# Performance work log

Measured on AMD Instinct MI355X. Metric: run time of the kernel, lower is better.

## Reference

```python
import jax, jax.numpy as jnp
import numpy as np

EPS_LOG = 1e-8
EPS_CHECK = 1e-4


def to_float8(x, exp_bits=4, mant_bits=3):
    # fp8 emulation: sign/abs/log2/floor/clamp/round chain
    max_exp = 2 ** (exp_bits - 1) - 1
    min_exp = -max_exp
    scale = 2.0 ** mant_bits
    sign = jnp.sign(x)
    x_abs = jnp.abs(x)
    exp = jnp.clip(jnp.floor(jnp.log2(x_abs + EPS_LOG)), min_exp, max_exp)
    pow2 = jnp.exp2(exp)
    mant = x_abs / pow2 - 1.0
    mant_q = jnp.round(mant * scale) / scale
    return sign * (1.0 + mant_q) * pow2


def checksum_verify(left, right, epsilon=EPS_CHECK):
    # ABFT: augment left with a column-sum row, right with a row-sum column
    left_cs = jnp.concatenate([left, jnp.sum(left, axis=0, keepdims=True)], axis=0)
    right_cs = jnp.concatenate([right, jnp.sum(right, axis=1, keepdims=True)], axis=1)
    prod_cs = left_cs @ right_cs  # [(m+1), (n+1)]
    output = prod_cs[:-1, :-1]
    row_sum_check = prod_cs[:-1, -1]
    col_sum_check = prod_cs[-1, :-1]
    col_diff = jnp.abs(jnp.sum(output, axis=0) - col_sum_check)
    row_diff = jnp.abs(jnp.sum(output, axis=1) - row_sum_check)
    mask = (row_diff > epsilon)[:, None] & (col_diff > epsilon)[None, :]
    return output, mask


def setup_inputs() -> dict:
    key = jax.random.key(0)
    kx, ku, kA, kB, kC = jax.random.split(key, 5)
    batch, n, m, p = 4096, 2048, 1024, 1024
    return {
        "x": jax.random.normal(kx, (batch, n), dtype=jnp.float32),
        "u": jax.random.normal(ku, (batch, m), dtype=jnp.float32),
        "A": jax.random.normal(kA, (n, n), dtype=jnp.float32),
        "B": jax.random.normal(kB, (n, m), dtype=jnp.float32),
        "C": jax.random.normal(kC, (p, n), dtype=jnp.float32),
    }


def reference(x, u, A, B, C):
    int_bits, frac_bits = 4, 3
    Aq = to_float8(A, int_bits, frac_bits)
    Bq = to_float8(B, int_bits, frac_bits)
    left_term, left_mask = checksum_verify(x, Aq.T)
    right_term, right_mask = checksum_verify(u, Bq.T)
    x_next = to_float8(left_term + right_term, int_bits, frac_bits)
    _ = left_mask | right_mask  # mask computed but discarded in forward (as in torch)
    Cq = to_float8(C, int_bits, frac_bits)
    y = to_float8(x_next @ Cq.T, int_bits, frac_bits)
    return (x_next, y)
```

## Files before the change

kernel.cpp:

```cpp
#include <hip/hip_runtime.h>
#include <hip/hip_bf16.h>
#include <stdint.h>

typedef __bf16 bf16_t;
typedef __attribute__((ext_vector_type(8))) __bf16 bf16x8;
typedef __attribute__((ext_vector_type(4))) __bf16 bf16x4;
typedef __attribute__((ext_vector_type(4))) float f32x4;

__device__ __forceinline__ float q8(float v) {
    float a = __builtin_fabsf(v);
    float z = a + 1e-8f;
    int ei = ((__float_as_int(z) >> 23) & 0xff) - 127;
    ei = ei > 7 ? 7 : (ei < -7 ? -7 : ei);
    float p  = __int_as_float((ei + 127) << 23);
    float ip = __int_as_float((127 - ei) << 23);
    float m  = __builtin_fmaf(a, ip, -1.0f);
    float mq = __builtin_rintf(m * 8.0f) * 0.125f;
    float r  = (1.0f + mq) * p;
    return v < 0.0f ? -r : r;
}

__device__ __forceinline__ void gload_lds16(const bf16_t* g, bf16_t* l) {
    __builtin_amdgcn_global_load_lds(
        (__attribute__((address_space(1))) void*)(g),
        (__attribute__((address_space(3))) void*)(l), 16, 0, 0);
}

__global__ void pack_all(const float* __restrict__ x, const float* __restrict__ u,
                         const float* __restrict__ A, const float* __restrict__ B,
                         const float* __restrict__ C,
                         bf16_t* __restrict__ XU, bf16_t* __restrict__ AB,
                         bf16_t* __restrict__ CQ) {
    int z = blockIdx.z;
    int row = blockIdx.y;
    int col = (blockIdx.x * 256 + threadIdx.x) * 4;
    if (z == 0) {
        float4 v;
        if (col < 2048) v = *(const float4*)&x[(size_t)row * 2048 + col];
        else            v = *(const float4*)&u[(size_t)row * 1024 + (col - 2048)];
        bf16x4 o = { (bf16_t)v.x, (bf16_t)v.y, (bf16_t)v.z, (bf16_t)v.w };
        *(bf16x4*)&XU[(size_t)row * 3072 + col] = o;
    } else if (z == 1) {
        if (row >= 2048) return;
        float4 v;
        if (col < 2048) v = *(const float4*)&A[(size_t)row * 2048 + col];
        else            v = *(const float4*)&B[(size_t)row * 1024 + (col - 2048)];
        bf16x4 o = { (bf16_t)q8(v.x), (bf16_t)q8(v.y), (bf16_t)q8(v.z), (bf16_t)q8(v.w) };
        *(bf16x4*)&AB[(size_t)row * 3072 + col] = o;
    } else {
        if (row >= 1024 || col >= 2048) return;
        float4 v = *(const float4*)&C[(size_t)row * 2048 + col];
        bf16x4 o = { (bf16_t)q8(v.x), (bf16_t)q8(v.y), (bf16_t)q8(v.z), (bf16_t)q8(v.w) };
        *(bf16x4*)&CQ[(size_t)row * 2048 + col] = o;
    }
}

template<int BN, bool DUAL>
__global__ __launch_bounds__(512, 4)
void gemm_q8_kernel(const bf16_t* __restrict__ A, const bf16_t* __restrict__ B,
                    float* __restrict__ outf, bf16_t* __restrict__ outb,
                    int M, int N, int K) {
    constexpr int BM = 128;
    constexpr int BK = 64;
    constexpr int NI = BN / 32;
    constexpr int A_ITS = BM * BK * 2 / 16 / 512;
    constexpr int B_ITS = BN * BK * 2 / 16 / 512;

    __shared__ alignas(16) bf16_t sA[BM * BK];
    __shared__ alignas(16) bf16_t sB[BN * BK];

    const int tid  = threadIdx.x;
    const int lane = tid & 63;
    const int wave = tid >> 6;
    const int wm   = wave & 3;
    const int wn   = wave >> 2;
    const int ln16 = lane & 15;
    const int quad = lane >> 4;

    const int brow = blockIdx.y * BM;
    const int bcol = blockIdx.x * BN;

    const bf16_t* gA[A_ITS]; bf16_t* lA[A_ITS];
#pragma unroll
    for (int it = 0; it < A_ITS; ++it) {
        int chunk = it * 512 + tid;
        int r  = chunk >> 3;
        int cg = (chunk & 7) ^ (r & 7);
        gA[it] = A + (size_t)(brow + r) * K + cg * 8;
        lA[it] = sA + (it * 512 + wave * 64) * 8;
    }
    const bf16_t* gB[B_ITS]; bf16_t* lB[B_ITS];
#pragma unroll
    for (int it = 0; it < B_ITS; ++it) {
        int chunk = it * 512 + tid;
        int r  = chunk >> 3;
        int cg = (chunk & 7) ^ (r & 7);
        gB[it] = B + (size_t)(bcol + r) * K + cg * 8;
        lB[it] = sB + (it * 512 + wave * 64) * 8;
    }

    int a_off[2][2], b_off[NI][2];
#pragma unroll
    for (int im = 0; im < 2; ++im) {
        int r = wm * 32 + im * 16 + ln16;
#pragma unroll
        for (int s = 0; s < 2; ++s) {
            int cg = s * 4 + quad;
            a_off[im][s] = (r * 8 + (cg ^ (r & 7))) * 8;
        }
    }
#pragma unroll
    for (int in = 0; in < NI; ++in) {
        int r = wn * (BN / 2) + in * 16 + ln16;
#pragma unroll
        for (int s = 0; s < 2; ++s) {
            int cg = s * 4 + quad;
            b_off[in][s] = (r * 8 + (cg ^ (r & 7))) * 8;
        }
    }

    f32x4 acc[2][NI];
#pragma unroll
    for (int im = 0; im < 2; ++im)
#pragma unroll
        for (int in = 0; in < NI; ++in)
            acc[im][in] = (f32x4){0.f, 0.f, 0.f, 0.f};

    for (int kt = 0; kt < K; kt += BK) {
#pragma unroll
        for (int it = 0; it < A_ITS; ++it) gload_lds16(gA[it], lA[it]);
#pragma unroll
        for (int it = 0; it < B_ITS; ++it) gload_lds16(gB[it], lB[it]);
#pragma unroll
        for (int it = 0; it < A_ITS; ++it) gA[it] += BK;
#pragma unroll
        for (int it = 0; it < B_ITS; ++it) gB[it] += BK;
        __syncthreads();
#pragma unroll
        for (int s = 0; s < 2; ++s) {
            bf16x8 af[2], bfv[NI];
#pragma unroll
            for (int im = 0; im < 2; ++im) af[im]  = *(const bf16x8*)(sA + a_off[im][s]);
#pragma unroll
            for (int in = 0; in < NI; ++in) bfv[in] = *(const bf16x8*)(sB + b_off[in][s]);
#pragma unroll
            for (int im = 0; im < 2; ++im)
#pragma unroll
                for (int in = 0; in < NI; ++in)
                    acc[im][in] = __builtin_amdgcn_mfma_f32_16x16x32_bf16(
                        af[im], bfv[in], acc[im][in], 0, 0, 0);
        }
        __syncthreads();
    }

    const int rbase = quad * 4;
#pragma unroll
    for (int im = 0; im < 2; ++im) {
#pragma unroll
        for (int in = 0; in < NI; ++in) {
            int gm = brow + wm * 32 + im * 16 + rbase;
            int gn = bcol + wn * (BN / 2) + in * 16 + ln16;
#pragma unroll
            for (int r = 0; r < 4; ++r) {
                float v = q8(acc[im][in][r]);
                outf[(size_t)(gm + r) * N + gn] = v;
                if (DUAL) outb[(size_t)(gm + r) * N + gn] = (bf16_t)v;
            }
        }
    }
}

extern "C" void kernel_launch(void* const* d_in, const int* in_sizes, int n_in,
                              void* d_out, int out_size, void* d_ws, size_t ws_size,
                              hipStream_t stream) {
    const float* x = (const float*)d_in[0];
    const float* u = (const float*)d_in[1];
    const float* A = (const float*)d_in[2];
    const float* B = (const float*)d_in[3];
    const float* C = (const float*)d_in[4];

    float* outf = (float*)d_out;
    float* xnf  = outf;
    float* yf   = outf + (size_t)4096 * 2048;

    uint8_t* ws = (uint8_t*)d_ws;
    bf16_t* XU = (bf16_t*)ws;
    bf16_t* AB = (bf16_t*)(ws + (size_t)25165824);
    bf16_t* CQ = (bf16_t*)(ws + (size_t)25165824 + 12582912);
    bf16_t* XN = (bf16_t*)(ws + (size_t)25165824 + 12582912 + 4194304);

    pack_all<<<dim3(3, 4096, 3), 256, 0, stream>>>(x, u, A, B, C, XU, AB, CQ);

    gemm_q8_kernel<128, true><<<dim3(2048 / 128, 4096 / 128), 512, 0, stream>>>(
        XU, AB, xnf, XN, 4096, 2048, 3072);
    gemm_q8_kernel<64, false><<<dim3(1024 / 64, 4096 / 128), 512, 0, stream>>>(
        XN, CQ, yf, nullptr, 4096, 1024, 2048);
}
```

Before: 218.8 us.

## Double GEMM K-tile to 128 and flatten pack grid to skip idle blocks

The GEMM K tile grows from 64 to 128, with the XOR swizzle widened to 16 column groups to match the larger row stride. This halves the number of barrier pairs per K loop and doubles the MFMA work between syncs, at the cost of twice the LDS per block, which may lower occupancy. Separately, the pack kernel's 3D grid, where many z=1/z=2 blocks returned immediately, becomes a 1D grid sized to exactly the useful blocks. That avoids launching empty workgroups.

```diff
diff --git a/kernel.cpp b/kernel.cpp
--- a/kernel.cpp
+++ b/kernel.cpp
@@ -31,24 +31,28 @@
                          const float* __restrict__ C,
                          bf16_t* __restrict__ XU, bf16_t* __restrict__ AB,
                          bf16_t* __restrict__ CQ) {
-    int z = blockIdx.z;
-    int row = blockIdx.y;
-    int col = (blockIdx.x * 256 + threadIdx.x) * 4;
-    if (z == 0) {
+    unsigned bid = blockIdx.x;
+    if (bid < 12288u) {
+        unsigned row = bid / 3u, piece = bid - row * 3u;
+        int col = (piece * 256 + threadIdx.x) * 4;
         float4 v;
         if (col < 2048) v = *(const float4*)&x[(size_t)row * 2048 + col];
         else            v = *(const float4*)&u[(size_t)row * 1024 + (col - 2048)];
         bf16x4 o = { (bf16_t)v.x, (bf16_t)v.y, (bf16_t)v.z, (bf16_t)v.w };
         *(bf16x4*)&XU[(size_t)row * 3072 + col] = o;
-    } else if (z == 1) {
-        if (row >= 2048) return;
+    } else if (bid < 18432u) {
+        unsigned b = bid - 12288u;
+        unsigned row = b / 3u, piece = b - row * 3u;
+        int col = (piece * 256 + threadIdx.x) * 4;
         float4 v;
         if (col < 2048) v = *(const float4*)&A[(size_t)row * 2048 + col];
         else            v = *(const float4*)&B[(size_t)row * 1024 + (col - 2048)];
         bf16x4 o = { (bf16_t)q8(v.x), (bf16_t)q8(v.y), (bf16_t)q8(v.z), (bf16_t)q8(v.w) };
         *(bf16x4*)&AB[(size_t)row * 3072 + col] = o;
     } else {
-        if (row >= 1024 || col >= 2048) return;
+        unsigned b = bid - 18432u;
+        unsigned row = b >> 1, piece = b & 1u;
+        int col = (piece * 256 + threadIdx.x) * 4;
         float4 v = *(const float4*)&C[(size_t)row * 2048 + col];
         bf16x4 o = { (bf16_t)q8(v.x), (bf16_t)q8(v.y), (bf16_t)q8(v.z), (bf16_t)q8(v.w) };
         *(bf16x4*)&CQ[(size_t)row * 2048 + col] = o;
@@ -61,10 +65,10 @@
                     float* __restrict__ outf, bf16_t* __restrict__ outb,
                     int M, int N, int K) {
     constexpr int BM = 128;
-    constexpr int BK = 64;
+    constexpr int BK = 128;
     constexpr int NI = BN / 32;
-    constexpr int A_ITS = BM * BK * 2 / 16 / 512;
-    constexpr int B_ITS = BN * BK * 2 / 16 / 512;
+    constexpr int A_ITS = BM * (BK / 8) / 512;
+    constexpr int B_ITS = BN * (BK / 8) / 512;
 
     __shared__ alignas(16) bf16_t sA[BM * BK];
     __shared__ alignas(16) bf16_t sB[BN * BK];
@@ -83,39 +87,37 @@
     const bf16_t* gA[A_ITS]; bf16_t* lA[A_ITS];
 #pragma unroll
     for (int it = 0; it < A_ITS; ++it) {
-        int chunk = it * 512 + tid;
-        int r  = chunk >> 3;
-        int cg = (chunk & 7) ^ (r & 7);
-        gA[it] = A + (size_t)(brow + r) * K + cg * 8;
+        int L = it * 512 + tid;
+        int r = L >> 4, c = L & 15;
+        gA[it] = A + (size_t)(brow + r) * K + (c ^ (r & 15)) * 8;
         lA[it] = sA + (it * 512 + wave * 64) * 8;
     }
     const bf16_t* gB[B_ITS]; bf16_t* lB[B_ITS];
 #pragma unroll
     for (int it = 0; it < B_ITS; ++it) {
-        int chunk = it * 512 + tid;
-        int r  = chunk >> 3;
-        int cg = (chunk & 7) ^ (r & 7);
-        gB[it] = B + (size_t)(bcol + r) * K + cg * 8;
+        int L = it * 512 + tid;
+        int r = L >> 4, c = L & 15;
+        gB[it] = B + (size_t)(bcol + r) * K + (c ^ (r & 15)) * 8;
         lB[it] = sB + (it * 512 + wave * 64) * 8;
     }
 
-    int a_off[2][2], b_off[NI][2];
+    int a_off[2][4], b_off[NI][4];
 #pragma unroll
     for (int im = 0; im < 2; ++im) {
         int r = wm * 32 + im * 16 + ln16;
 #pragma unroll
-        for (int s = 0; s < 2; ++s) {
+        for (int s = 0; s < 4; ++s) {
             int cg = s * 4 + quad;
-            a_off[im][s] = (r * 8 + (cg ^ (r & 7))) * 8;
+            a_off[im][s] = (r * 16 + (cg ^ (r & 15))) * 8;
         }
     }
 #pragma unroll
     for (int in = 0; in < NI; ++in) {
         int r = wn * (BN / 2) + in * 16 + ln16;
 #pragma unroll
-        for (int s = 0; s < 2; ++s) {
+        for (int s = 0; s < 4; ++s) {
             int cg = s * 4 + quad;
-            b_off[in][s] = (r * 8 + (cg ^ (r & 7))) * 8;
+            b_off[in][s] = (r * 16 + (cg ^ (r & 15))) * 8;
         }
     }
 
@@ -137,7 +139,7 @@
         for (int it = 0; it < B_ITS; ++it) gB[it] += BK;
         __syncthreads();
 #pragma unroll
-        for (int s = 0; s < 2; ++s) {
+        for (int s = 0; s < 4; ++s) {
             bf16x8 af[2], bfv[NI];
 #pragma unroll
             for (int im = 0; im < 2; ++im) af[im]  = *(const bf16x8*)(sA + a_off[im][s]);
@@ -189,7 +191,7 @@
     bf16_t* CQ = (bf16_t*)(ws + (size_t)25165824 + 12582912);
     bf16_t* XN = (bf16_t*)(ws + (size_t)25165824 + 12582912 + 4194304);
 
-    pack_all<<<dim3(3, 4096, 3), 256, 0, stream>>>(x, u, A, B, C, XU, AB, CQ);
+    pack_all<<<dim3(20480), 256, 0, stream>>>(x, u, A, B, C, XU, AB, CQ);
 
     gemm_q8_kernel<128, true><<<dim3(2048 / 128, 4096 / 128), 512, 0, stream>>>(
         XU, AB, xnf, XN, 4096, 2048, 3072);
```

Measured after the change: 203.3 us. 7.1% less time.
